# Performance work log

Measured on AMD Instinct MI355X. Metric: run time of the kernel, lower is better.

The kernel has to match this reference:

```python
import jax, jax.numpy as jnp
from jax import lax
import numpy as np

# ---- geometry constants (from metadata / module __init__) ----
NA = 1152            # rotview (number of projection angles)
ND = 736             # det_count
NP = 512             # reconstructed image size
VOX = 1.0 / 0.7      # vox_scaling
D   = VOX * 595.0    # source-to-isocenter distance
DD  = VOX * 490.6    # isocenter-to-detector distance
DU  = VOX * 1.2858   # detector pixel spacing
DSD = D + DD         # source-to-detector distance
ANGLES = np.linspace(0.0, 2.0 * np.pi, NA, endpoint=False) + np.pi / 2.0

# ---- Shepp-Logan Fourier filter (skimage/torch-radon construction) ----
PAD = max(64, int(2 ** np.ceil(np.log2(2 * ND))))  # 2048

def _shepp_logan_filter(size):
    n = np.concatenate([np.arange(1, size // 2 + 1, 2),
                        np.arange(size // 2 - 1, 0, -2)])
    f = np.zeros(size)
    f[0] = 0.25
    f[1::2] = -1.0 / (np.pi * n) ** 2
    four = 2.0 * np.real(np.fft.fft(f))            # ramp filter
    omega = np.pi * np.fft.fftfreq(size)[1:]
    four[1:] *= np.sin(omega) / omega              # Shepp-Logan window
    return four[: size // 2 + 1].astype(np.float32)  # rfft half-spectrum

FILT = jnp.asarray(_shepp_logan_filter(PAD))
COS_A = jnp.asarray(np.cos(ANGLES).astype(np.float32))
SIN_A = jnp.asarray(np.sin(ANGLES).astype(np.float32))


def _filter_sinogram(sino):
    # sino: (NA, ND). Zero-pad to PAD, filter in Fourier domain, crop.
    padded = jnp.pad(sino, ((0, 0), (0, PAD - ND)))
    spec = jnp.fft.rfft(padded, axis=-1) * FILT
    filt = jnp.fft.irfft(spec, n=PAD, axis=-1)[:, :ND]
    return filt * (np.pi / (2.0 * NA))


def _backproject(filtered):
    # Pixel-driven fan-beam (flat detector) backprojection.
    c = (NP - 1) / 2.0
    coords = jnp.arange(NP, dtype=jnp.float32) - c
    ys, xs = jnp.meshgrid(coords, coords, indexing='ij')  # (NP, NP)

    def body(acc, inp):
        cb, sb, row = inp
        pdot = xs * cb + ys * sb            # pixel coord along source dir
        pe = -xs * sb + ys * cb             # pixel coord along detector axis
        den = D - pdot                      # source->pixel depth
        u = DSD * pe / den                  # detector coordinate (mm)
        iu = u / DU + (ND - 1) / 2.0        # fractional detector index
        i0 = jnp.floor(iu)
        frac = iu - i0
        i0i = i0.astype(jnp.int32)
        valid = (i0i >= 0) & (i0i < ND - 1) & (den > 0)
        i0c = jnp.clip(i0i, 0, ND - 2)
        v = row[i0c] * (1.0 - frac) + row[i0c + 1] * frac  # linear interp
        w = (D / den) ** 2                   # fan-beam distance weighting
        return acc + jnp.where(valid, w * v, 0.0), None

    img, _ = lax.scan(body, jnp.zeros((NP, NP), jnp.float32),
                      (COS_A, SIN_A, filtered))
    return img


def setup_inputs() -> dict:
    key = jax.random.key(0)
    x = jax.random.normal(key, (1, 1, NA, ND), dtype=jnp.float32)
    return {"x": x}


def reference(x):
    sino = x[0, 0]                          # (NA, ND) after squeeze
    filtered = _filter_sinogram(sino)
    fbp = _backproject(filtered)
    # mu -> HU -> normalize to [0, 1] window
    fbp_hu = (1000.0 * ((fbp - 0.0192) / 0.0192) - (-1024.0)) / (3072.0 - (-1024.0))
    return fbp_hu[None, None]               # (1, 1, 512, 512)
```

## Files before the change

### kernel.cpp

```cpp
#include <hip/hip_runtime.h>
#include <math.h>

#ifndef M_PI
#define M_PI 3.14159265358979323846
#endif

#define NAANG 1152
#define NDET  736
#define NPIX  512
#define PADN  2048
#define NHALF 1025

#define OFF_FILTD 0
#define OFF_H     8320
#define OFF_TRIG  16512
#define OFF_FS    34944
#define OFF_PART  3426432

typedef float f32x2 __attribute__((ext_vector_type(2)));

static __device__ __forceinline__ f32x2 load2(const float* p) {
    f32x2 r;
    __builtin_memcpy(&r, p, 8);
    return r;
}

__global__ void filt_spec_kernel(double* __restrict__ filt_d) {
    __shared__ double red[256];
    const int m = blockIdx.x;
    const int t = threadIdx.x;
    double s = 0.0;
    for (int j = t; j < 1024; j += 256) {
        int n = (j < 512) ? (2 * j + 1) : (2047 - 2 * j);
        double fj = -1.0 / ((M_PI * n) * (M_PI * n));
        double ang = (2.0 * M_PI) * (double)m * (double)(2 * j + 1) / (double)PADN;
        s += fj * cos(ang);
    }
    red[t] = s;
    __syncthreads();
    for (int w = 128; w > 0; w >>= 1) {
        if (t < w) red[t] += red[t + w];
        __syncthreads();
    }
    if (t == 0) {
        double four = 2.0 * (0.25 + red[0]);
        if (m > 0) {
            double om = M_PI * (double)m / (double)PADN;
            four *= sin(om) / om;
        }
        filt_d[m] = four;
    }
}

__global__ void h_kernel(const double* __restrict__ filt_d, float* __restrict__ h,
                         float4* __restrict__ trig) {
    __shared__ double red[256];
    const int k = blockIdx.x;
    const int t = threadIdx.x;
    if (t == 0 && k < NAANG) {
        double ang = 2.0 * M_PI * (double)k / (double)NAANG + M_PI / 2.0;
        double c = cos(ang), s = sin(ang);
        double K = 1085.6 / 1.2858;
        trig[k] = make_float4((float)c, (float)s, (float)(K * c), (float)(K * s));
    }
    double s = 0.0;
    for (int m = t; m <= 1024; m += 256) {
        double c;
        if (m == 0) c = 1.0;
        else if (m == 1024) c = (k & 1) ? -1.0 : 1.0;
        else c = 2.0 * cos((2.0 * M_PI) * (double)m * (double)k / (double)PADN);
        s += filt_d[m] * c;
    }
    red[t] = s;
    __syncthreads();
    for (int w = 128; w > 0; w >>= 1) {
        if (t < w) red[t] += red[t + w];
        __syncthreads();
    }
    if (t == 0)
        h[k] = (float)(red[0] / (double)PADN * (M_PI / (2.0 * (double)NAANG)));
}

__global__ void conv_kernel(const float* __restrict__ x,
                            const float* __restrict__ h,
                            float* __restrict__ fs) {
    __shared__ float sh2[2816];
    __shared__ float srow[NDET];
    const int row = blockIdx.x;
    const int t = threadIdx.x;
    const float4* h4 = (const float4*)h;
    for (int i = t; i < 704; i += 192) ((float4*)sh2)[i] = h4[i & 511];
    const float4* x4 = (const float4*)(x + row * NDET);
    for (int i = t; i < NDET / 4; i += 192) ((float4*)srow)[i] = x4[i];
    __syncthreads();

    const int t4 = 4 * t;
    float o0 = 0.f, o1 = 0.f, o2 = 0.f, o3 = 0.f;
    #pragma unroll 2
    for (int j = 0; j < NDET; j += 4) {
        float4 r4 = *(const float4*)&srow[j];
        const int A = t4 + PADN - j;
        float4 hlo = *(const float4*)&sh2[A - 4];
        float4 hhi = *(const float4*)&sh2[A];
        o0 = fmaf(r4.x, hhi.x, o0); o0 = fmaf(r4.y, hlo.w, o0);
        o0 = fmaf(r4.z, hlo.z, o0); o0 = fmaf(r4.w, hlo.y, o0);
        o1 = fmaf(r4.x, hhi.y, o1); o1 = fmaf(r4.y, hhi.x, o1);
        o1 = fmaf(r4.z, hlo.w, o1); o1 = fmaf(r4.w, hlo.z, o1);
        o2 = fmaf(r4.x, hhi.z, o2); o2 = fmaf(r4.y, hhi.y, o2);
        o2 = fmaf(r4.z, hhi.x, o2); o2 = fmaf(r4.w, hlo.w, o2);
        o3 = fmaf(r4.x, hhi.w, o3); o3 = fmaf(r4.y, hhi.z, o3);
        o3 = fmaf(r4.z, hhi.y, o3); o3 = fmaf(r4.w, hhi.x, o3);
    }
    if (t < NDET / 4)
        *(float4*)&fs[row * NDET + t4] = make_float4(o0, o1, o2, o3);
}

template<int NCH>
__global__ __launch_bounds__(256, 8)
void backproj_kernel(const float* __restrict__ fs,
                     const float4* __restrict__ trig,
                     float* __restrict__ partial) {
    constexpr int ACL = NAANG / NCH;
    __shared__ float4 st[ACL];
    const int t = threadIdx.x;
    const int abase = blockIdx.z * ACL;
    for (int i = t; i < ACL; i += 256) st[i] = trig[abase + i];
    __syncthreads();

    const int ix = blockIdx.x * 256 + t;
    const int iy = blockIdx.y * 4;
    const float xs  = (float)ix - 255.5f;
    const float ys0 = (float)iy - 255.5f;
    const float Dg = 850.0f;

    const float* rowp = fs + (size_t)abase * NDET;
    float acc0 = 0.f, acc1 = 0.f, acc2 = 0.f, acc3 = 0.f;
    for (int a = 0; a < ACL; ++a, rowp += NDET) {
        float4 q = st[a];
        float sb2 = q.y + q.y;
        float kc2 = q.z + q.z;
        float den0 = fmaf(-xs, q.x, fmaf(-ys0, q.y, Dg));
        float kpe0 = fmaf(ys0, q.z, -(xs * q.w));
        float den1 = den0 - q.y, den2 = den0 - sb2, den3 = den2 - q.y;
        float kpe1 = kpe0 + q.z, kpe2 = kpe0 + kc2, kpe3 = kpe2 + q.z;

        float r0 = __builtin_amdgcn_rcpf(den0);
        float r1 = __builtin_amdgcn_rcpf(den1);
        float r2 = __builtin_amdgcn_rcpf(den2);
        float r3 = __builtin_amdgcn_rcpf(den3);
        float iu0 = fmaf(kpe0, r0, 367.5f);
        float iu1 = fmaf(kpe1, r1, 367.5f);
        float iu2 = fmaf(kpe2, r2, 367.5f);
        float iu3 = fmaf(kpe3, r3, 367.5f);
        float f0 = floorf(iu0), f1 = floorf(iu1), f2 = floorf(iu2), f3 = floorf(iu3);
        int   i0 = (int)f0, i1 = (int)f1, i2 = (int)f2, i3 = (int)f3;
        int   c0 = min(max(i0, 0), NDET - 2);
        int   c1 = min(max(i1, 0), NDET - 2);
        int   c2 = min(max(i2, 0), NDET - 2);
        int   c3 = min(max(i3, 0), NDET - 2);
        f32x2 g0 = load2(rowp + c0);
        f32x2 g1 = load2(rowp + c1);
        f32x2 g2 = load2(rowp + c2);
        f32x2 g3 = load2(rowp + c3);
        float fr0 = iu0 - f0, fr1 = iu1 - f1, fr2 = iu2 - f2, fr3 = iu3 - f3;
        float v0 = fmaf(fr0, g0.y - g0.x, g0.x);
        float v1 = fmaf(fr1, g1.y - g1.x, g1.x);
        float v2 = fmaf(fr2, g2.y - g2.x, g2.x);
        float v3 = fmaf(fr3, g3.y - g3.x, g3.x);
        float d0 = Dg * r0, d1 = Dg * r1, d2 = Dg * r2, d3 = Dg * r3;
        float w0 = d0 * d0, w1 = d1 * d1, w2 = d2 * d2, w3 = d3 * d3;
        w0 = ((unsigned)i0 < (unsigned)(NDET - 1)) ? w0 : 0.f;
        w1 = ((unsigned)i1 < (unsigned)(NDET - 1)) ? w1 : 0.f;
        w2 = ((unsigned)i2 < (unsigned)(NDET - 1)) ? w2 : 0.f;
        w3 = ((unsigned)i3 < (unsigned)(NDET - 1)) ? w3 : 0.f;
        acc0 = fmaf(w0, v0, acc0);
        acc1 = fmaf(w1, v1, acc1);
        acc2 = fmaf(w2, v2, acc2);
        acc3 = fmaf(w3, v3, acc3);
    }
    float* outp = partial + ((size_t)blockIdx.z * NPIX + iy) * NPIX + ix;
    outp[0 * NPIX] = acc0;
    outp[1 * NPIX] = acc1;
    outp[2 * NPIX] = acc2;
    outp[3 * NPIX] = acc3;
}

template<int NCH>
__global__ void combine_kernel(const float* __restrict__ partial,
                               float* __restrict__ out) {
    int p = blockIdx.x * 256 + threadIdx.x;
    float s = 0.f;
    #pragma unroll
    for (int c = 0; c < NCH; ++c) s += partial[c * NPIX * NPIX + p];
    out[p] = fmaf(s, (float)(1000.0 / 0.0192 / 4096.0), 0.005859375f);
}

extern "C" void kernel_launch(void* const* d_in, const int* in_sizes, int n_in,
                              void* d_out, int out_size, void* d_ws, size_t ws_size,
                              hipStream_t stream) {
    const float* x = (const float*)d_in[0];
    float* out = (float*)d_out;

    char* ws = (char*)d_ws;
    double* filt_d = (double*)(ws + OFF_FILTD);
    float*  h      = (float*)(ws + OFF_H);
    float4* trig   = (float4*)(ws + OFF_TRIG);
    float*  fs     = (float*)(ws + OFF_FS);
    float*  part   = (float*)(ws + OFF_PART);

    filt_spec_kernel<<<NHALF, 256, 0, stream>>>(filt_d);
    h_kernel<<<PADN, 256, 0, stream>>>(filt_d, h, trig);
    conv_kernel<<<NAANG, 192, 0, stream>>>(x, h, fs);

    const size_t pbytes = (size_t)NPIX * NPIX * 4;
    if (ws_size >= OFF_PART + 8 * pbytes) {
        backproj_kernel<8><<<dim3(2, 128, 8), 256, 0, stream>>>(fs, trig, part);
        combine_kernel<8><<<NPIX * NPIX / 256, 256, 0, stream>>>(part, out);
    } else if (ws_size >= OFF_PART + 4 * pbytes) {
        backproj_kernel<4><<<dim3(2, 128, 4), 256, 0, stream>>>(fs, trig, part);
        combine_kernel<4><<<NPIX * NPIX / 256, 256, 0, stream>>>(part, out);
    } else if (ws_size >= OFF_PART + 2 * pbytes) {
        backproj_kernel<2><<<dim3(2, 128, 2), 256, 0, stream>>>(fs, trig, part);
        combine_kernel<2><<<NPIX * NPIX / 256, 256, 0, stream>>>(part, out);
    } else {
        backproj_kernel<1><<<dim3(2, 128, 1), 256, 0, stream>>>(fs, trig, part);
        combine_kernel<1><<<NPIX * NPIX / 256, 256, 0, stream>>>(part, out);
    }
}
```

Before: 265.1 us.

## Use float trig in filter setup, 2-row conv, LDS-staged backprojection rows

The filter-spectrum and impulse-response kernels move from double to float arithmetic, using cospif with exact integer phase reduction. The convolution processes two sinogram rows per block with eight outputs per thread to raise register reuse of the filter taps. The backprojection stages two detector rows at a time in double-buffered shared memory with register prefetch, so the interpolation gathers hit LDS instead of global memory. This costs a block barrier per angle pair and some precision in the filter construction.

Measured after the change: 279.8 us. 1.06x slower.

```diff
diff --git a/kernel.cpp b/kernel.cpp
--- a/kernel.cpp
+++ b/kernel.cpp
@@ -11,30 +11,24 @@
 #define PADN  2048
 #define NHALF 1025
 
-#define OFF_FILTD 0
-#define OFF_H     8320
-#define OFF_TRIG  16512
-#define OFF_FS    34944
-#define OFF_PART  3426432
+#define OFF_FILTF 0
+#define OFF_H     4224
+#define OFF_TRIG  12416
+#define OFF_FS    30848
+#define OFF_PART  3422336
 
 typedef float f32x2 __attribute__((ext_vector_type(2)));
 
-static __device__ __forceinline__ f32x2 load2(const float* p) {
-    f32x2 r;
-    __builtin_memcpy(&r, p, 8);
-    return r;
-}
-
-__global__ void filt_spec_kernel(double* __restrict__ filt_d) {
-    __shared__ double red[256];
+__global__ void filt_spec_kernel(float* __restrict__ filt_f) {
+    __shared__ float red[256];
     const int m = blockIdx.x;
     const int t = threadIdx.x;
-    double s = 0.0;
+    float s = 0.f;
     for (int j = t; j < 1024; j += 256) {
         int n = (j < 512) ? (2 * j + 1) : (2047 - 2 * j);
-        double fj = -1.0 / ((M_PI * n) * (M_PI * n));
-        double ang = (2.0 * M_PI) * (double)m * (double)(2 * j + 1) / (double)PADN;
-        s += fj * cos(ang);
+        float fj = (float)(-1.0 / ((M_PI * n) * (M_PI * n)));
+        int r = (m * (2 * j + 1)) & (PADN - 1);
+        s += fj * cospif((float)r * (1.0f / 1024.0f));
     }
     red[t] = s;
     __syncthreads();
@@ -43,18 +37,18 @@
         __syncthreads();
     }
     if (t == 0) {
-        double four = 2.0 * (0.25 + red[0]);
+        double four = 2.0 * (0.25 + (double)red[0]);
         if (m > 0) {
             double om = M_PI * (double)m / (double)PADN;
             four *= sin(om) / om;
         }
-        filt_d[m] = four;
-    }
-}
-
-__global__ void h_kernel(const double* __restrict__ filt_d, float* __restrict__ h,
-                         float4* __restrict__ trig) {
-    __shared__ double red[256];
+        filt_f[m] = (float)four;
+    }
+}
+
+__global__ void h_kernel(const float* __restrict__ filt_f,
+                         float* __restrict__ h, float4* __restrict__ trig) {
+    __shared__ float red[256];
     const int k = blockIdx.x;
     const int t = threadIdx.x;
     if (t == 0 && k < NAANG) {
@@ -63,13 +57,14 @@
         double K = 1085.6 / 1.2858;
         trig[k] = make_float4((float)c, (float)s, (float)(K * c), (float)(K * s));
     }
-    double s = 0.0;
+    float s = 0.f;
     for (int m = t; m <= 1024; m += 256) {
-        double c;
-        if (m == 0) c = 1.0;
-        else if (m == 1024) c = (k & 1) ? -1.0 : 1.0;
-        else c = 2.0 * cos((2.0 * M_PI) * (double)m * (double)k / (double)PADN);
-        s += filt_d[m] * c;
+        float F = filt_f[m];
+        float c;
+        if (m == 0) c = 1.f;
+        else if (m == 1024) c = (k & 1) ? -1.f : 1.f;
+        else c = 2.f * cospif((float)((m * k) & (PADN - 1)) * (1.0f / 1024.0f));
+        s += F * c;
     }
     red[t] = s;
     __syncthreads();
@@ -78,41 +73,51 @@
         __syncthreads();
     }
     if (t == 0)
-        h[k] = (float)(red[0] / (double)PADN * (M_PI / (2.0 * (double)NAANG)));
+        h[k] = (float)((double)red[0] / (double)PADN * (M_PI / (2.0 * (double)NAANG)));
 }
 
 __global__ void conv_kernel(const float* __restrict__ x,
                             const float* __restrict__ h,
                             float* __restrict__ fs) {
     __shared__ float sh2[2816];
-    __shared__ float srow[NDET];
-    const int row = blockIdx.x;
-    const int t = threadIdx.x;
+    __shared__ float srow[2][NDET];
+    const int t = threadIdx.x;
+    const int row0 = blockIdx.x * 2;
     const float4* h4 = (const float4*)h;
     for (int i = t; i < 704; i += 192) ((float4*)sh2)[i] = h4[i & 511];
-    const float4* x4 = (const float4*)(x + row * NDET);
-    for (int i = t; i < NDET / 4; i += 192) ((float4*)srow)[i] = x4[i];
-    __syncthreads();
-
-    const int t4 = 4 * t;
-    float o0 = 0.f, o1 = 0.f, o2 = 0.f, o3 = 0.f;
+    const float4* x4 = (const float4*)(x + (size_t)row0 * NDET);
+    for (int i = t; i < 368; i += 192) ((float4*)srow[0])[i] = x4[i];
+    __syncthreads();
+
+    const int r = t / 96;
+    const int u = t % 96;
+    const float* my = srow[r];
+    const int A0 = 8 * u + PADN;
+    float o[8] = {0.f, 0.f, 0.f, 0.f, 0.f, 0.f, 0.f, 0.f};
     #pragma unroll 2
-    for (int j = 0; j < NDET; j += 4) {
-        float4 r4 = *(const float4*)&srow[j];
-        const int A = t4 + PADN - j;
-        float4 hlo = *(const float4*)&sh2[A - 4];
-        float4 hhi = *(const float4*)&sh2[A];
-        o0 = fmaf(r4.x, hhi.x, o0); o0 = fmaf(r4.y, hlo.w, o0);
-        o0 = fmaf(r4.z, hlo.z, o0); o0 = fmaf(r4.w, hlo.y, o0);
-        o1 = fmaf(r4.x, hhi.y, o1); o1 = fmaf(r4.y, hhi.x, o1);
-        o1 = fmaf(r4.z, hlo.w, o1); o1 = fmaf(r4.w, hlo.z, o1);
-        o2 = fmaf(r4.x, hhi.z, o2); o2 = fmaf(r4.y, hhi.y, o2);
-        o2 = fmaf(r4.z, hhi.x, o2); o2 = fmaf(r4.w, hlo.w, o2);
-        o3 = fmaf(r4.x, hhi.w, o3); o3 = fmaf(r4.y, hhi.z, o3);
-        o3 = fmaf(r4.z, hhi.y, o3); o3 = fmaf(r4.w, hhi.x, o3);
-    }
-    if (t < NDET / 4)
-        *(float4*)&fs[row * NDET + t4] = make_float4(o0, o1, o2, o3);
+    for (int j = 0; j < NDET; j += 8) {
+        float4 s0 = *(const float4*)&my[j];
+        float4 s1 = *(const float4*)&my[j + 4];
+        const float* hp = &sh2[A0 - j - 8];
+        float4 h0 = *(const float4*)(hp);
+        float4 h1 = *(const float4*)(hp + 4);
+        float4 h2 = *(const float4*)(hp + 8);
+        float4 h3 = *(const float4*)(hp + 12);
+        float wv[16] = {h0.x, h0.y, h0.z, h0.w, h1.x, h1.y, h1.z, h1.w,
+                        h2.x, h2.y, h2.z, h2.w, h3.x, h3.y, h3.z, h3.w};
+        float se[8]  = {s0.x, s0.y, s0.z, s0.w, s1.x, s1.y, s1.z, s1.w};
+        #pragma unroll
+        for (int e = 0; e < 8; ++e) {
+            #pragma unroll
+            for (int d = 0; d < 8; ++d)
+                o[d] = fmaf(se[e], wv[8 + d - e], o[d]);
+        }
+    }
+    if (u < 92) {
+        float* op = fs + (size_t)(row0 + r) * NDET + 8 * u;
+        *(float4*)op       = make_float4(o[0], o[1], o[2], o[3]);
+        *(float4*)(op + 4) = make_float4(o[4], o[5], o[6], o[7]);
+    }
 }
 
 template<int NCH>
@@ -121,10 +126,18 @@
                      const float4* __restrict__ trig,
                      float* __restrict__ partial) {
     constexpr int ACL = NAANG / NCH;
+    constexpr int NG  = ACL / 2;
     __shared__ float4 st[ACL];
+    __shared__ float rows[2][2 * NDET];
     const int t = threadIdx.x;
     const int abase = blockIdx.z * ACL;
     for (int i = t; i < ACL; i += 256) st[i] = trig[abase + i];
+    {
+        const float4* src = (const float4*)(fs + (size_t)abase * NDET);
+        float4* dst = (float4*)rows[0];
+        dst[t] = src[t];
+        if (t < 112) dst[t + 256] = src[t + 256];
+    }
     __syncthreads();
 
     const int ix = blockIdx.x * 256 + t;
@@ -133,50 +146,67 @@
     const float ys0 = (float)iy - 255.5f;
     const float Dg = 850.0f;
 
-    const float* rowp = fs + (size_t)abase * NDET;
     float acc0 = 0.f, acc1 = 0.f, acc2 = 0.f, acc3 = 0.f;
-    for (int a = 0; a < ACL; ++a, rowp += NDET) {
-        float4 q = st[a];
-        float sb2 = q.y + q.y;
-        float kc2 = q.z + q.z;
-        float den0 = fmaf(-xs, q.x, fmaf(-ys0, q.y, Dg));
-        float kpe0 = fmaf(ys0, q.z, -(xs * q.w));
-        float den1 = den0 - q.y, den2 = den0 - sb2, den3 = den2 - q.y;
-        float kpe1 = kpe0 + q.z, kpe2 = kpe0 + kc2, kpe3 = kpe2 + q.z;
-
-        float r0 = __builtin_amdgcn_rcpf(den0);
-        float r1 = __builtin_amdgcn_rcpf(den1);
-        float r2 = __builtin_amdgcn_rcpf(den2);
-        float r3 = __builtin_amdgcn_rcpf(den3);
-        float iu0 = fmaf(kpe0, r0, 367.5f);
-        float iu1 = fmaf(kpe1, r1, 367.5f);
-        float iu2 = fmaf(kpe2, r2, 367.5f);
-        float iu3 = fmaf(kpe3, r3, 367.5f);
-        float f0 = floorf(iu0), f1 = floorf(iu1), f2 = floorf(iu2), f3 = floorf(iu3);
-        int   i0 = (int)f0, i1 = (int)f1, i2 = (int)f2, i3 = (int)f3;
-        int   c0 = min(max(i0, 0), NDET - 2);
-        int   c1 = min(max(i1, 0), NDET - 2);
-        int   c2 = min(max(i2, 0), NDET - 2);
-        int   c3 = min(max(i3, 0), NDET - 2);
-        f32x2 g0 = load2(rowp + c0);
-        f32x2 g1 = load2(rowp + c1);
-        f32x2 g2 = load2(rowp + c2);
-        f32x2 g3 = load2(rowp + c3);
-        float fr0 = iu0 - f0, fr1 = iu1 - f1, fr2 = iu2 - f2, fr3 = iu3 - f3;
-        float v0 = fmaf(fr0, g0.y - g0.x, g0.x);
-        float v1 = fmaf(fr1, g1.y - g1.x, g1.x);
-        float v2 = fmaf(fr2, g2.y - g2.x, g2.x);
-        float v3 = fmaf(fr3, g3.y - g3.x, g3.x);
-        float d0 = Dg * r0, d1 = Dg * r1, d2 = Dg * r2, d3 = Dg * r3;
-        float w0 = d0 * d0, w1 = d1 * d1, w2 = d2 * d2, w3 = d3 * d3;
-        w0 = ((unsigned)i0 < (unsigned)(NDET - 1)) ? w0 : 0.f;
-        w1 = ((unsigned)i1 < (unsigned)(NDET - 1)) ? w1 : 0.f;
-        w2 = ((unsigned)i2 < (unsigned)(NDET - 1)) ? w2 : 0.f;
-        w3 = ((unsigned)i3 < (unsigned)(NDET - 1)) ? w3 : 0.f;
-        acc0 = fmaf(w0, v0, acc0);
-        acc1 = fmaf(w1, v1, acc1);
-        acc2 = fmaf(w2, v2, acc2);
-        acc3 = fmaf(w3, v3, acc3);
+    for (int g = 0; g < NG; ++g) {
+        float4 p0, p1;
+        const bool pf = (g + 1 < NG);
+        if (pf) {
+            const float4* src =
+                (const float4*)(fs + (size_t)(abase + 2 * (g + 1)) * NDET);
+            p0 = src[t];
+            if (t < 112) p1 = src[t + 256];
+        }
+        const float* bufb = rows[g & 1];
+        #pragma unroll
+        for (int gg = 0; gg < 2; ++gg) {
+            const float* row = bufb + gg * NDET;
+            float4 q = st[2 * g + gg];
+            float sb2 = q.y + q.y, kc2 = q.z + q.z;
+            float den0 = fmaf(-xs, q.x, fmaf(-ys0, q.y, Dg));
+            float kpe0 = fmaf(ys0, q.z, -(xs * q.w));
+            float den1 = den0 - q.y, den2 = den0 - sb2, den3 = den2 - q.y;
+            float kpe1 = kpe0 + q.z, kpe2 = kpe0 + kc2, kpe3 = kpe2 + q.z;
+            float r0 = __builtin_amdgcn_rcpf(den0);
+            float r1 = __builtin_amdgcn_rcpf(den1);
+            float r2 = __builtin_amdgcn_rcpf(den2);
+            float r3 = __builtin_amdgcn_rcpf(den3);
+            float iu0 = fmaf(kpe0, r0, 367.5f);
+            float iu1 = fmaf(kpe1, r1, 367.5f);
+            float iu2 = fmaf(kpe2, r2, 367.5f);
+            float iu3 = fmaf(kpe3, r3, 367.5f);
+            float f0 = floorf(iu0), f1 = floorf(iu1);
+            float f2 = floorf(iu2), f3 = floorf(iu3);
+            int i0 = (int)f0, i1 = (int)f1, i2 = (int)f2, i3 = (int)f3;
+            int c0 = min(max(i0, 0), NDET - 2);
+            int c1 = min(max(i1, 0), NDET - 2);
+            int c2 = min(max(i2, 0), NDET - 2);
+            int c3 = min(max(i3, 0), NDET - 2);
+            float a0 = row[c0], b0 = row[c0 + 1];
+            float a1 = row[c1], b1 = row[c1 + 1];
+            float a2 = row[c2], b2 = row[c2 + 1];
+            float a3 = row[c3], b3 = row[c3 + 1];
+            float fr0 = iu0 - f0, fr1 = iu1 - f1;
+            float fr2 = iu2 - f2, fr3 = iu3 - f3;
+            float v0 = fmaf(fr0, b0 - a0, a0);
+            float v1 = fmaf(fr1, b1 - a1, a1);
+            float v2 = fmaf(fr2, b2 - a2, a2);
+            float v3 = fmaf(fr3, b3 - a3, a3);
+            float d0 = Dg * r0, d1 = Dg * r1, d2 = Dg * r2, d3 = Dg * r3;
+            float w0 = ((unsigned)i0 < (unsigned)(NDET - 1)) ? d0 * d0 : 0.f;
+            float w1 = ((unsigned)i1 < (unsigned)(NDET - 1)) ? d1 * d1 : 0.f;
+            float w2 = ((unsigned)i2 < (unsigned)(NDET - 1)) ? d2 * d2 : 0.f;
+            float w3 = ((unsigned)i3 < (unsigned)(NDET - 1)) ? d3 * d3 : 0.f;
+            acc0 = fmaf(w0, v0, acc0);
+            acc1 = fmaf(w1, v1, acc1);
+            acc2 = fmaf(w2, v2, acc2);
+            acc3 = fmaf(w3, v3, acc3);
+        }
+        if (pf) {
+            float4* dst = (float4*)rows[(g + 1) & 1];
+            dst[t] = p0;
+            if (t < 112) dst[t + 256] = p1;
+        }
+        __syncthreads();
     }
     float* outp = partial + ((size_t)blockIdx.z * NPIX + iy) * NPIX + ix;
     outp[0 * NPIX] = acc0;
@@ -202,15 +232,15 @@
     float* out = (float*)d_out;
 
     char* ws = (char*)d_ws;
-    double* filt_d = (double*)(ws + OFF_FILTD);
+    float*  filt_f = (float*)(ws + OFF_FILTF);
     float*  h      = (float*)(ws + OFF_H);
     float4* trig   = (float4*)(ws + OFF_TRIG);
     float*  fs     = (float*)(ws + OFF_FS);
     float*  part   = (float*)(ws + OFF_PART);
 
-    filt_spec_kernel<<<NHALF, 256, 0, stream>>>(filt_d);
-    h_kernel<<<PADN, 256, 0, stream>>>(filt_d, h, trig);
-    conv_kernel<<<NAANG, 192, 0, stream>>>(x, h, fs);
+    filt_spec_kernel<<<NHALF, 256, 0, stream>>>(filt_f);
+    h_kernel<<<PADN, 256, 0, stream>>>(filt_f, h, trig);
+    conv_kernel<<<NAANG / 2, 192, 0, stream>>>(x, h, fs);
 
     const size_t pbytes = (size_t)NPIX * NPIX * 4;
     if (ws_size >= OFF_PART + 8 * pbytes) {
```
